# Kernel tuning notes

Hardware: AMD Instinct MI355X
Metric: run time of the kernel (lower is better)

Reference implementation:

```python
import jax, jax.numpy as jnp
import numpy as np

B, H, W, DIM = 32, 56, 56, 192
WSZ = 7
HEADS = 8
DK = 32
DV = 32
INNER_K = HEADS * DK  # 256
INNER_V = HEADS * DV  # 256


def setup_inputs() -> dict:
    key = jax.random.key(0)
    ks = jax.random.split(key, 8)
    s = 0.05
    return {
        "x": jax.random.normal(ks[0], (B, H, W, DIM), jnp.float32),
        "Wq": jax.random.normal(ks[1], (DIM, INNER_K), jnp.float32) * s,
        "Wk": jax.random.normal(ks[2], (DIM, INNER_K), jnp.float32) * s,
        "Wv": jax.random.normal(ks[3], (DIM, INNER_V), jnp.float32) * s,
        "Wlocal": jax.random.normal(ks[4], (3, 3, INNER_V, INNER_V), jnp.float32) * s,
        "b_local": jnp.zeros((INNER_V,), jnp.float32),
        "Wout": jax.random.normal(ks[5], (INNER_V, DIM), jnp.float32) * s,
        "b_out": jnp.zeros((DIM,), jnp.float32),
    }


def _window(t, heads, wsz):
    # (b, H, W, heads*d) -> (b*nx*ny, heads, wsz*wsz, d)
    b, h, w, c = t.shape
    d = c // heads
    nx, ny = h // wsz, w // wsz
    t = t.reshape(b, nx, wsz, ny, wsz, heads, d)
    t = t.transpose(0, 1, 3, 5, 2, 4, 6)
    return t.reshape(b * nx * ny, heads, wsz * wsz, d)


def reference(x, Wq, Wk, Wv, Wlocal, b_local, Wout, b_out):
    scale = DK ** (-0.5)
    # 1x1 convs == per-pixel matmuls
    q = jnp.einsum('bhwc,cd->bhwd', x, Wq)
    k = jnp.einsum('bhwc,cd->bhwd', x, Wk)
    v = jnp.einsum('bhwc,cd->bhwd', x, Wv)
    # 3x3 local interactive conv on v (SAME padding)
    local_out = jax.lax.conv_general_dilated(
        v, Wlocal, window_strides=(1, 1), padding='SAME',
        dimension_numbers=('NHWC', 'HWIO', 'NHWC')) + b_local
    # window partition
    qw = _window(q, HEADS, WSZ)
    kw = _window(k, HEADS, WSZ)
    vw = _window(v, HEADS, WSZ)
    dots = jnp.einsum('bhid,bhjd->bhij', qw, kw) * scale  # (B*nx*ny, heads, 49, 49)
    attn = jax.nn.softmax(dots, axis=-1)
    out = jnp.einsum('bhij,bhjd->bhid', attn, vw)
    # window merge: (b*nx*ny, heads, wsz*wsz, d) -> (b, H, W, heads*d)
    nx, ny = H // WSZ, W // WSZ
    out = out.reshape(B, nx, ny, HEADS, WSZ, WSZ, DV)
    out = out.transpose(0, 1, 4, 2, 5, 3, 6).reshape(B, H, W, HEADS * DV)
    out = out + local_out
    out = jnp.einsum('bhwc,cd->bhwd', out, Wout) + b_out
    return out
```

## Files before the change

kernel.cpp:

```cpp
#include <hip/hip_runtime.h>

typedef unsigned short ushort_t;
typedef __bf16  bf16x8 __attribute__((ext_vector_type(8)));
typedef float   f32x4  __attribute__((ext_vector_type(4)));
typedef unsigned short u16x8 __attribute__((ext_vector_type(8)));

#define MFMA16(a,b,c) __builtin_amdgcn_mfma_f32_16x16x32_bf16((a),(b),(c),0,0,0)
#define WAITVM(N) asm volatile("s_waitcnt vmcnt(" #N ")" ::: "memory")
#define BARRIER() do{ __builtin_amdgcn_s_barrier(); asm volatile("" ::: "memory"); }while(0)

static __device__ __forceinline__ ushort_t f2bf(float f){
  __bf16 h = (__bf16)f;
  return __builtin_bit_cast(ushort_t, h);
}
static __device__ __forceinline__ float bf2f(ushort_t b){
  union{unsigned u; float f;} x; x.u = ((unsigned)b)<<16; return x.f;
}
static __device__ __forceinline__ bf16x8 ldg_bf8u(const ushort_t* p){
  u16x8 r = *(const u16x8*)p;
  return __builtin_bit_cast(bf16x8, r);
}
static __device__ __forceinline__ bf16x8 lds_bf8(const ushort_t* p){
  u16x8 r = *(const u16x8*)p;
  return __builtin_bit_cast(bf16x8, r);
}
static __device__ __forceinline__ void gload_lds16(const ushort_t* g, ushort_t* l){
  __builtin_amdgcn_global_load_lds(
      (const __attribute__((address_space(1))) void*)g,
      (__attribute__((address_space(3))) void*)l, 16, 0, 0);
}

__global__ __launch_bounds__(256) void prep_kernel(
    const float* __restrict__ Wq, const float* __restrict__ Wk,
    const float* __restrict__ Wv, const float* __restrict__ Wl,
    const float* __restrict__ Wo,
    ushort_t* __restrict__ qkvT, ushort_t* __restrict__ wlT,
    ushort_t* __restrict__ woT)
{
  int idx = blockIdx.x*256 + threadIdx.x;
  if(idx < 147456){
    int n = idx/192, kk = idx%192;
    const float* W = (n < 256) ? Wq : ((n < 512) ? Wk : Wv);
    qkvT[idx] = f2bf(W[kk*256 + (n & 255)]);
  } else if(idx < 147456 + 589824){
    int t2 = idx - 147456;
    int j   = t2 & 7;
    int sl  = (t2 >> 3) & 3;
    int col = (t2 >> 5) & 255;
    int ks  = (t2 >> 13) & 7;
    int tap = t2 >> 16;
    int grp = sl ^ ((col>>1)&3);
    int k = ks*32 + grp*8 + j;
    wlT[t2] = f2bf(Wl[((size_t)tap*256 + k)*256 + col]);
  } else if(idx < 737280 + 49152){
    int t3 = idx - 737280;
    int col = t3/256, kk = t3%256;
    woT[t3] = f2bf(Wo[kk*192 + col]);
  }
}

__global__ __launch_bounds__(256,2) void qkvattn_kernel(
    const float* __restrict__ x, const ushort_t* __restrict__ WT,
    ushort_t* __restrict__ vbuf, ushort_t* __restrict__ attnout)
{
  __shared__ ushort_t lds[38912];
  ushort_t* xLds = lds;
  const int tid = threadIdx.x;
  const int w = tid>>6, l = tid&63, lr = l&15, g = l>>4;
  const int bid = blockIdx.x;
  const int win = bid>>1, head = (bid&1)*4 + w;
  const int b = win>>6, rem = win&63, wy = rem>>3, wx = rem&7;
  const size_t base = (size_t)b*3136 + wy*7*56 + wx*7;

  #pragma unroll
  for(int r=0;r<6;++r){
    int c = tid + r*256;
    int row = c/24, cp = c%24;
    if(row < 49){
      int sc = cp ^ (row&7);
      const float* src = x + (base + (row/7)*56 + (row%7))*192 + sc*8;
      float4 f0 = *(const float4*)src;
      float4 f1 = *(const float4*)(src+4);
      u16x8 o;
      o[0]=f2bf(f0.x); o[1]=f2bf(f0.y); o[2]=f2bf(f0.z); o[3]=f2bf(f0.w);
      o[4]=f2bf(f1.x); o[5]=f2bf(f1.y); o[6]=f2bf(f1.z); o[7]=f2bf(f1.w);
      *(u16x8*)&xLds[row*192 + cp*8] = o;
    } else {
      u16x8 z = {0,0,0,0,0,0,0,0};
      *(u16x8*)&xLds[row*192 + cp*8] = z;
    }
  }
  __syncthreads();

  ushort_t* qkBase = lds + 12288 + w*4608;
  ushort_t* vT     = lds + 30720 + w*2048;
  const ushort_t* Wq_ = WT + (size_t)(head*32)*192;
  const ushort_t* Wk_ = WT + (size_t)(256 + head*32)*192;
  const ushort_t* Wv_ = WT + (size_t)(512 + head*32)*192;

  {
    f32x4 aq[4][2], ak[4][2];
    #pragma unroll
    for(int mi=0;mi<4;++mi)
      #pragma unroll
      for(int nj=0;nj<2;++nj){
        f32x4 z={0.f,0.f,0.f,0.f};
        aq[mi][nj]=z; ak[mi][nj]=z;
      }
    #pragma unroll
    for(int ks=0; ks<6; ++ks){
      bf16x8 af[4];
      #pragma unroll
      for(int mi=0;mi<4;++mi){
        int row = mi*16 + lr;
        af[mi] = lds_bf8(&xLds[(row*192 + ks*32 + g*8) ^ ((row&7)<<3)]);
      }
      bf16x8 bq[2], bk[2];
      #pragma unroll
      for(int nj=0;nj<2;++nj){
        size_t off = (size_t)(nj*16+lr)*192 + ks*32 + g*8;
        bq[nj] = ldg_bf8u(Wq_ + off);
        bk[nj] = ldg_bf8u(Wk_ + off);
      }
      #pragma unroll
      for(int nj=0;nj<2;++nj)
        #pragma unroll
        for(int mi=0;mi<4;++mi){
          aq[mi][nj] = MFMA16(af[mi], bq[nj], aq[mi][nj]);
          ak[mi][nj] = MFMA16(af[mi], bk[nj], ak[mi][nj]);
        }
    }
    #pragma unroll
    for(int mi=0;mi<4;++mi)
      #pragma unroll
      for(int nj=0;nj<2;++nj)
        #pragma unroll
        for(int i=0;i<4;++i){
          int row = mi*16 + g*4 + i, col = nj*16 + lr;
          qkBase[row*36 + col]        = f2bf(aq[mi][nj][i]);
          qkBase[2304 + row*36 + col] = f2bf(ak[mi][nj][i]);
        }
  }

  {
    f32x4 av[4][2];
    #pragma unroll
    for(int mi=0;mi<4;++mi)
      #pragma unroll
      for(int nj=0;nj<2;++nj){ f32x4 z={0.f,0.f,0.f,0.f}; av[mi][nj]=z; }
    #pragma unroll
    for(int ks=0; ks<6; ++ks){
      bf16x8 af[4];
      #pragma unroll
      for(int mi=0;mi<4;++mi){
        int row = mi*16 + lr;
        af[mi] = lds_bf8(&xLds[(row*192 + ks*32 + g*8) ^ ((row&7)<<3)]);
      }
      bf16x8 bv[2];
      #pragma unroll
      for(int nj=0;nj<2;++nj)
        bv[nj] = ldg_bf8u(Wv_ + (size_t)(nj*16+lr)*192 + ks*32 + g*8);
      #pragma unroll
      for(int nj=0;nj<2;++nj)
        #pragma unroll
        for(int mi=0;mi<4;++mi)
          av[mi][nj] = MFMA16(af[mi], bv[nj], av[mi][nj]);
    }
    #pragma unroll
    for(int mi=0;mi<4;++mi)
      #pragma unroll
      for(int nj=0;nj<2;++nj)
        #pragma unroll
        for(int i=0;i<4;++i){
          int row = mi*16 + g*4 + i, col = nj*16 + lr;
          ushort_t val = f2bf(av[mi][nj][i]);
          vT[(col*64 + row) ^ ((col&7)<<3)] = val;
          if(row < 49)
            vbuf[(base + (row/7)*56 + (row%7))*256 + head*32 + col] = val;
        }
  }

  f32x4 dot[4][4];
  #pragma unroll
  for(int mi=0;mi<4;++mi)
    #pragma unroll
    for(int nj=0;nj<4;++nj){ f32x4 z={0.f,0.f,0.f,0.f}; dot[mi][nj]=z; }
  bf16x8 qf[4], kf[4];
  #pragma unroll
  for(int t=0;t<4;++t){
    qf[t] = lds_bf8(&qkBase[(t*16+lr)*36 + g*8]);
    kf[t] = lds_bf8(&qkBase[2304 + (t*16+lr)*36 + g*8]);
  }
  #pragma unroll
  for(int mi=0;mi<4;++mi)
    #pragma unroll
    for(int nj=0;nj<4;++nj)
      dot[mi][nj] = MFMA16(qf[mi], kf[nj], dot[mi][nj]);

  const float sc = 0.17677669529663687f * 1.4426950408889634f;
  ushort_t* pl = qkBase;
  #pragma unroll
  for(int mi=0;mi<4;++mi)
    #pragma unroll
    for(int nj=0;nj<4;++nj){
      int col = nj*16 + lr;
      #pragma unroll
      for(int i=0;i<4;++i){
        float e = (col < 49) ? exp2f(dot[mi][nj][i]*sc) : 0.f;
        int row = mi*16 + g*4 + i;
        pl[(row*64 + col) ^ ((row&7)<<3)] = f2bf(e);
      }
    }

  u16x8 ones_u = {0x3f80,0x3f80,0x3f80,0x3f80,0x3f80,0x3f80,0x3f80,0x3f80};
  bf16x8 ones8 = __builtin_bit_cast(bf16x8, ones_u);
  f32x4 o[4][2], rsum[4];
  #pragma unroll
  for(int mi=0;mi<4;++mi){
    f32x4 z={0.f,0.f,0.f,0.f};
    o[mi][0]=z; o[mi][1]=z; rsum[mi]=z;
  }
  #pragma unroll
  for(int ks=0;ks<2;++ks){
    bf16x8 pa[4];
    #pragma unroll
    for(int mi=0;mi<4;++mi){
      int row = mi*16 + lr;
      pa[mi] = lds_bf8(&pl[(row*64 + ks*32 + g*8) ^ ((row&7)<<3)]);
    }
    #pragma unroll
    for(int nj=0;nj<2;++nj){
      int d = nj*16 + lr;
      bf16x8 vb = lds_bf8(&vT[(d*64 + ks*32 + g*8) ^ ((d&7)<<3)]);
      #pragma unroll
      for(int mi=0;mi<4;++mi) o[mi][nj] = MFMA16(pa[mi], vb, o[mi][nj]);
    }
    #pragma unroll
    for(int mi=0;mi<4;++mi) rsum[mi] = MFMA16(pa[mi], ones8, rsum[mi]);
  }
  #pragma unroll
  for(int mi=0;mi<4;++mi){
    #pragma unroll
    for(int i=0;i<4;++i){
      int row = mi*16 + g*4 + i;
      if(row < 49){
        size_t pix = base + (row/7)*56 + (row%7);
        float inv = 1.0f / rsum[mi][i];
        #pragma unroll
        for(int nj=0;nj<2;++nj)
          attnout[pix*256 + head*32 + nj*16 + lr] = f2bf(o[mi][nj][i] * inv);
      }
    }
  }
}

__global__ __launch_bounds__(256,2) void conv_kernel(
    const ushort_t* __restrict__ v, const ushort_t* __restrict__ WlT,
    const float* __restrict__ b_local, ushort_t* __restrict__ local_out)
{
  __shared__ ushort_t aBuf[2][256*32];
  __shared__ ushort_t bBuf[3][256*32];
  const int bid = blockIdx.x;
  const int tile = (bid & 7) * 98 + (bid >> 3);
  const int p0 = tile * 128;
  const int tid = threadIdx.x;
  const int l = tid&63, w=tid>>6, wm=w>>1, wn=w&1, lr=l&15, g=l>>4;

  unsigned maskbits[4];
  int pxloc[4];
  #pragma unroll
  for(int mi=0;mi<4;++mi){
    int p = p0 + wm*64 + mi*16 + lr;
    int rem = p % 3136;
    int y = rem/56, x = rem%56;
    unsigned mb = 0;
    #pragma unroll
    for(int tap=0;tap<9;++tap){
      int dy = tap/3 - 1, dx = tap%3 - 1;
      if(((unsigned)(y+dy) < 56u) && ((unsigned)(x+dx) < 56u)) mb |= (1u<<tap);
    }
    maskbits[mi] = mb;
    pxloc[mi] = wm*64 + mi*16 + lr + 64;
  }

  auto stageA = [&](int ks, ushort_t* dst){
    #pragma unroll
    for(int r=0;r<4;++r){
      int c = tid + r*256;
      int px = c>>2, sl = c&3;
      int px_abs = p0 - 64 + px;
      px_abs = min(max(px_abs, 0), 100351);
      int chunk = sl ^ ((px>>1)&3);
      gload_lds16(v + (size_t)px_abs*256 + ks*32 + chunk*8,
                  dst + (size_t)(r*256 + w*64)*8);
    }
  };
  auto stageB = [&](int ks, int tap, ushort_t* dst){
    const ushort_t* src = WlT + ((size_t)tap*8 + ks)*8192;
    #pragma unroll
    for(int r=0;r<4;++r){
      gload_lds16(src + (size_t)(tid + r*256)*8,
                  dst + (size_t)(r*256 + w*64)*8);
    }
  };

  f32x4 acc[4][8];
  #pragma unroll
  for(int mi=0;mi<4;++mi)
    #pragma unroll
    for(int nj=0;nj<8;++nj){ f32x4 z={0.f,0.f,0.f,0.f}; acc[mi][nj]=z; }

  auto compute = [&](int tap, const ushort_t* aL, const ushort_t* bL){
    int shift = (tap/3 - 1)*56 + (tap%3 - 1);
    bf16x8 af[4];
    #pragma unroll
    for(int mi=0;mi<4;++mi){
      int px = pxloc[mi] + shift;
      int sl = g ^ ((px>>1)&3);
      u16x8 rv = *(const u16x8*)&aL[px*32 + sl*8];
      if(!((maskbits[mi]>>tap)&1)){ u16x8 z={0,0,0,0,0,0,0,0}; rv=z; }
      af[mi] = __builtin_bit_cast(bf16x8, rv);
    }
    __builtin_amdgcn_s_setprio(1);
    #pragma unroll
    for(int nj=0;nj<8;++nj){
      int col = wn*128 + nj*16 + lr;
      int slb = g ^ ((col>>1)&3);
      bf16x8 bfr = lds_bf8(&bL[col*32 + slb*8]);
      #pragma unroll
      for(int mi=0;mi<4;++mi) acc[mi][nj] = MFMA16(af[mi], bfr, acc[mi][nj]);
    }
    __builtin_amdgcn_s_setprio(0);
  };

  stageA(0, aBuf[0]);
  stageB(0, 0, bBuf[0]);
  stageB(0, 1, bBuf[1]);

  for(int ks=0; ks<7; ++ks){
    #pragma unroll
    for(int tap=0; tap<9; ++tap){
      if(tap==1) WAITVM(8); else WAITVM(4);
      BARRIER();
      if(tap==0) stageA(ks+1, aBuf[(ks+1)&1]);
      stageB(ks + (tap+2)/9, (tap+2)%9, bBuf[(tap+2)%3]);
      compute(tap, aBuf[ks&1], bBuf[tap%3]);
    }
  }
  #pragma unroll
  for(int tap=0; tap<9; ++tap){
    if(tap==8) WAITVM(0); else WAITVM(4);
    BARRIER();
    if(tap<7) stageB(7, tap+2, bBuf[(tap+2)%3]);
    compute(tap, aBuf[1], bBuf[tap%3]);
  }

  #pragma unroll
  for(int nj=0;nj<8;++nj){
    int col = wn*128 + nj*16 + lr;
    float bb = b_local[col];
    #pragma unroll
    for(int mi=0;mi<4;++mi)
      #pragma unroll
      for(int i=0;i<4;++i){
        int p = p0 + wm*64 + mi*16 + g*4 + i;
        local_out[(size_t)p*256 + col] = f2bf(acc[mi][nj][i] + bb);
      }
  }
}

__global__ __launch_bounds__(256,4) void outproj_kernel(
    const ushort_t* __restrict__ attnout, const ushort_t* __restrict__ locl,
    const ushort_t* __restrict__ WoT, const float* __restrict__ b_out,
    float* __restrict__ out)
{
  __shared__ ushort_t aLds[64*256];
  const int m0 = blockIdx.x * 64;
  const int tid = threadIdx.x;
  const int l = tid&63, w = tid>>6, lr=l&15, g=l>>4;
  #pragma unroll
  for(int r=0;r<8;++r){
    int c = tid + r*256;
    int row = c>>5, cc = c&31;
    size_t off = (size_t)(m0+row)*256 + cc*8;
    u16x8 a = *(const u16x8*)(attnout + off);
    u16x8 b2 = *(const u16x8*)(locl + off);
    u16x8 o;
    #pragma unroll
    for(int j=0;j<8;++j) o[j] = f2bf(bf2f(a[j]) + bf2f(b2[j]));
    *(u16x8*)&aLds[(row*256 + cc*8) ^ ((row&7)<<3)] = o;
  }
  __syncthreads();

  const ushort_t* Wbase = WoT + (size_t)(w*48)*256;
  f32x4 acc[4][3];
  #pragma unroll
  for(int mi=0;mi<4;++mi)
    #pragma unroll
    for(int nj=0;nj<3;++nj){ f32x4 z={0.f,0.f,0.f,0.f}; acc[mi][nj]=z; }

  #pragma unroll
  for(int ks=0;ks<8;++ks){
    bf16x8 bfr[3];
    #pragma unroll
    for(int nj=0;nj<3;++nj)
      bfr[nj] = ldg_bf8u(Wbase + (size_t)(nj*16+lr)*256 + ks*32 + g*8);
    bf16x8 af[4];
    #pragma unroll
    for(int mi=0;mi<4;++mi){
      int row = mi*16 + lr;
      af[mi] = lds_bf8(&aLds[(row*256 + ks*32 + g*8) ^ ((row&7)<<3)]);
    }
    #pragma unroll
    for(int nj=0;nj<3;++nj)
      #pragma unroll
      for(int mi=0;mi<4;++mi) acc[mi][nj] = MFMA16(af[mi], bfr[nj], acc[mi][nj]);
  }
  #pragma unroll
  for(int nj=0;nj<3;++nj){
    int col = w*48 + nj*16 + lr;
    float bb = b_out[col];
    #pragma unroll
    for(int mi=0;mi<4;++mi)
      #pragma unroll
      for(int i=0;i<4;++i){
        int row = mi*16 + g*4 + i;
        out[(size_t)(m0+row)*192 + col] = acc[mi][nj][i] + bb;
      }
  }
}

extern "C" void kernel_launch(void* const* d_in, const int* in_sizes, int n_in,
                              void* d_out, int out_size, void* d_ws, size_t ws_size,
                              hipStream_t stream)
{
  const float* x  = (const float*)d_in[0];
  const float* Wq = (const float*)d_in[1];
  const float* Wk = (const float*)d_in[2];
  const float* Wv = (const float*)d_in[3];
  const float* Wl = (const float*)d_in[4];
  const float* bl = (const float*)d_in[5];
  const float* Wo = (const float*)d_in[6];
  const float* bo = (const float*)d_in[7];
  float* out = (float*)d_out;
  char* ws = (char*)d_ws;
  ushort_t* attnout = (ushort_t*)(ws);
  ushort_t* vbuf    = (ushort_t*)(ws + 102760448);
  ushort_t* locl    = (ushort_t*)(ws + 205520896);
  ushort_t* qkvT    = (ushort_t*)(ws + 256901120);
  ushort_t* wlT     = (ushort_t*)(ws + 257196032);
  ushort_t* woT     = (ushort_t*)(ws + 258375680);

  prep_kernel<<<3072, 256, 0, stream>>>(Wq, Wk, Wv, Wl, Wo, qkvT, wlT, woT);
  qkvattn_kernel<<<4096, 256, 0, stream>>>(x, qkvT, vbuf, attnout);
  conv_kernel<<<784, 256, 0, stream>>>(vbuf, wlT, bl, locl);
  outproj_kernel<<<1568, 256, 0, stream>>>(attnout, locl, woT, bo, out);
}
```

Before: 323.5 us.

## Pre-convert x to bf16 in prep kernel and load A fragments from global

The fp32-to-bf16 conversion of x moves into the prep kernel, which now writes a bf16 copy of x to workspace. The QKV/attention kernel no longer stages the window into shared memory. Each wave instead loads its MFMA A fragments straight from the bf16 global buffer, clamping padded rows to row 48. This removes the LDS staging, its barrier and about 24KB of LDS per block, and halves the bytes of x each attention block reads. In exchange it adds a full extra write-and-read pass over x, and every wave now fetches x fragments redundantly from global/L2 instead of sharing them through LDS.

```diff
diff --git a/kernel.cpp b/kernel.cpp
--- a/kernel.cpp
+++ b/kernel.cpp
@@ -31,11 +31,12 @@
 }
 
 __global__ __launch_bounds__(256) void prep_kernel(
+    const float* __restrict__ x,
     const float* __restrict__ Wq, const float* __restrict__ Wk,
     const float* __restrict__ Wv, const float* __restrict__ Wl,
     const float* __restrict__ Wo,
     ushort_t* __restrict__ qkvT, ushort_t* __restrict__ wlT,
-    ushort_t* __restrict__ woT)
+    ushort_t* __restrict__ woT, ushort_t* __restrict__ xbf)
 {
   int idx = blockIdx.x*256 + threadIdx.x;
   if(idx < 147456){
@@ -56,15 +57,23 @@
     int t3 = idx - 737280;
     int col = t3/256, kk = t3%256;
     woT[t3] = f2bf(Wo[kk*192 + col]);
+  } else {
+    int c = idx - 786432;
+    const float* src = x + (size_t)c*8;
+    float4 f0 = *(const float4*)src;
+    float4 f1 = *(const float4*)(src+4);
+    u16x8 o;
+    o[0]=f2bf(f0.x); o[1]=f2bf(f0.y); o[2]=f2bf(f0.z); o[3]=f2bf(f0.w);
+    o[4]=f2bf(f1.x); o[5]=f2bf(f1.y); o[6]=f2bf(f1.z); o[7]=f2bf(f1.w);
+    *(u16x8*)&xbf[(size_t)c*8] = o;
   }
 }
 
 __global__ __launch_bounds__(256,2) void qkvattn_kernel(
-    const float* __restrict__ x, const ushort_t* __restrict__ WT,
+    const ushort_t* __restrict__ xbf, const ushort_t* __restrict__ WT,
     ushort_t* __restrict__ vbuf, ushort_t* __restrict__ attnout)
 {
-  __shared__ ushort_t lds[38912];
-  ushort_t* xLds = lds;
+  __shared__ ushort_t lds[26624];
   const int tid = threadIdx.x;
   const int w = tid>>6, l = tid&63, lr = l&15, g = l>>4;
   const int bid = blockIdx.x;
@@ -72,28 +81,15 @@
   const int b = win>>6, rem = win&63, wy = rem>>3, wx = rem&7;
   const size_t base = (size_t)b*3136 + wy*7*56 + wx*7;
 
-  #pragma unroll
-  for(int r=0;r<6;++r){
-    int c = tid + r*256;
-    int row = c/24, cp = c%24;
-    if(row < 49){
-      int sc = cp ^ (row&7);
-      const float* src = x + (base + (row/7)*56 + (row%7))*192 + sc*8;
-      float4 f0 = *(const float4*)src;
-      float4 f1 = *(const float4*)(src+4);
-      u16x8 o;
-      o[0]=f2bf(f0.x); o[1]=f2bf(f0.y); o[2]=f2bf(f0.z); o[3]=f2bf(f0.w);
-      o[4]=f2bf(f1.x); o[5]=f2bf(f1.y); o[6]=f2bf(f1.z); o[7]=f2bf(f1.w);
-      *(u16x8*)&xLds[row*192 + cp*8] = o;
-    } else {
-      u16x8 z = {0,0,0,0,0,0,0,0};
-      *(u16x8*)&xLds[row*192 + cp*8] = z;
-    }
-  }
-  __syncthreads();
-
-  ushort_t* qkBase = lds + 12288 + w*4608;
-  ushort_t* vT     = lds + 30720 + w*2048;
+  const ushort_t* aPtr[4];
+  #pragma unroll
+  for(int mi=0;mi<4;++mi){
+    int row = mi*16 + lr; row = (row > 48) ? 48 : row;
+    aPtr[mi] = xbf + (base + (row/7)*56 + (row%7))*192;
+  }
+
+  ushort_t* qkBase = lds + w*4608;
+  ushort_t* vT     = lds + 18432 + w*2048;
   const ushort_t* Wq_ = WT + (size_t)(head*32)*192;
   const ushort_t* Wk_ = WT + (size_t)(256 + head*32)*192;
   const ushort_t* Wv_ = WT + (size_t)(512 + head*32)*192;
@@ -111,10 +107,7 @@
     for(int ks=0; ks<6; ++ks){
       bf16x8 af[4];
       #pragma unroll
-      for(int mi=0;mi<4;++mi){
-        int row = mi*16 + lr;
-        af[mi] = lds_bf8(&xLds[(row*192 + ks*32 + g*8) ^ ((row&7)<<3)]);
-      }
+      for(int mi=0;mi<4;++mi) af[mi] = ldg_bf8u(aPtr[mi] + ks*32 + g*8);
       bf16x8 bq[2], bk[2];
       #pragma unroll
       for(int nj=0;nj<2;++nj){
@@ -152,10 +145,7 @@
     for(int ks=0; ks<6; ++ks){
       bf16x8 af[4];
       #pragma unroll
-      for(int mi=0;mi<4;++mi){
-        int row = mi*16 + lr;
-        af[mi] = lds_bf8(&xLds[(row*192 + ks*32 + g*8) ^ ((row&7)<<3)]);
-      }
+      for(int mi=0;mi<4;++mi) af[mi] = ldg_bf8u(aPtr[mi] + ks*32 + g*8);
       bf16x8 bv[2];
       #pragma unroll
       for(int nj=0;nj<2;++nj)
@@ -445,14 +435,15 @@
   float* out = (float*)d_out;
   char* ws = (char*)d_ws;
   ushort_t* attnout = (ushort_t*)(ws);
+  ushort_t* xbf     = (ushort_t*)(ws + 51380224);
   ushort_t* vbuf    = (ushort_t*)(ws + 102760448);
   ushort_t* locl    = (ushort_t*)(ws + 205520896);
   ushort_t* qkvT    = (ushort_t*)(ws + 256901120);
   ushort_t* wlT     = (ushort_t*)(ws + 257196032);
   ushort_t* woT     = (ushort_t*)(ws + 258375680);
 
-  prep_kernel<<<3072, 256, 0, stream>>>(Wq, Wk, Wv, Wl, Wo, qkvT, wlT, woT);
-  qkvattn_kernel<<<4096, 256, 0, stream>>>(x, qkvT, vbuf, attnout);
+  prep_kernel<<<12480, 256, 0, stream>>>(x, Wq, Wk, Wv, Wl, Wo, qkvT, wlT, woT, xbf);
+  qkvattn_kernel<<<4096, 256, 0, stream>>>(xbf, qkvT, vbuf, attnout);
   conv_kernel<<<784, 256, 0, stream>>>(vbuf, wlT, bl, locl);
   outproj_kernel<<<1568, 256, 0, stream>>>(attnout, locl, woT, bo, out);
 }
```

Measured after the change: 341.9 us. 5.7% more time.

## Fuse output projection into local conv kernel via shared-memory epilogue

Applied to the files above, without the earlier changes.

Merges the conv and out-projection kernels. Each conv block writes its 128x256 local output tile to shared memory, adds the attention output tile, then runs the Wout GEMM from shared memory and writes the final fp32 result. This removes the bf16 local_out round trip through global memory and one kernel launch. In exchange the conv kernel holds more accumulator registers at occupancy 2 and has a serial epilogue with extra barriers.

```diff
diff --git a/kernel.cpp b/kernel.cpp
--- a/kernel.cpp
+++ b/kernel.cpp
@@ -254,12 +254,16 @@
   }
 }
 
-__global__ __launch_bounds__(256,2) void conv_kernel(
+__global__ __launch_bounds__(256,2) void conv_outproj_kernel(
     const ushort_t* __restrict__ v, const ushort_t* __restrict__ WlT,
-    const float* __restrict__ b_local, ushort_t* __restrict__ local_out)
+    const ushort_t* __restrict__ attnout, const float* __restrict__ b_local,
+    const ushort_t* __restrict__ woT, const float* __restrict__ b_out,
+    float* __restrict__ out)
 {
-  __shared__ ushort_t aBuf[2][256*32];
-  __shared__ ushort_t bBuf[3][256*32];
+  __shared__ ushort_t sh[40960];
+  ushort_t* aBuf0 = sh;
+  ushort_t* aBuf1 = sh + 8192;
+  ushort_t* bBufs = sh + 16384;
   const int bid = blockIdx.x;
   const int tile = (bid & 7) * 98 + (bid >> 3);
   const int p0 = tile * 128;
@@ -333,28 +337,30 @@
     __builtin_amdgcn_s_setprio(0);
   };
 
-  stageA(0, aBuf[0]);
-  stageB(0, 0, bBuf[0]);
-  stageB(0, 1, bBuf[1]);
+  stageA(0, aBuf0);
+  stageB(0, 0, bBufs);
+  stageB(0, 1, bBufs + 8192);
 
   for(int ks=0; ks<7; ++ks){
     #pragma unroll
     for(int tap=0; tap<9; ++tap){
       if(tap==1) WAITVM(8); else WAITVM(4);
       BARRIER();
-      if(tap==0) stageA(ks+1, aBuf[(ks+1)&1]);
-      stageB(ks + (tap+2)/9, (tap+2)%9, bBuf[(tap+2)%3]);
-      compute(tap, aBuf[ks&1], bBuf[tap%3]);
+      if(tap==0) stageA(ks+1, (ks&1) ? aBuf0 : aBuf1);
+      stageB(ks + (tap+2)/9, (tap+2)%9, bBufs + ((tap+2)%3)*8192);
+      compute(tap, (ks&1) ? aBuf1 : aBuf0, bBufs + (tap%3)*8192);
     }
   }
   #pragma unroll
   for(int tap=0; tap<9; ++tap){
     if(tap==8) WAITVM(0); else WAITVM(4);
     BARRIER();
-    if(tap<7) stageB(7, tap+2, bBuf[(tap+2)%3]);
-    compute(tap, aBuf[1], bBuf[tap%3]);
-  }
-
+    if(tap<7) stageB(7, tap+2, bBufs + ((tap+2)%3)*8192);
+    compute(tap, aBuf1, bBufs + (tap%3)*8192);
+  }
+
+  BARRIER();
+  ushort_t* sum = sh;
   #pragma unroll
   for(int nj=0;nj<8;++nj){
     int col = wn*128 + nj*16 + lr;
@@ -363,69 +369,56 @@
     for(int mi=0;mi<4;++mi)
       #pragma unroll
       for(int i=0;i<4;++i){
-        int p = p0 + wm*64 + mi*16 + g*4 + i;
-        local_out[(size_t)p*256 + col] = f2bf(acc[mi][nj][i] + bb);
-      }
-  }
-}
-
-__global__ __launch_bounds__(256,4) void outproj_kernel(
-    const ushort_t* __restrict__ attnout, const ushort_t* __restrict__ locl,
-    const ushort_t* __restrict__ WoT, const float* __restrict__ b_out,
-    float* __restrict__ out)
-{
-  __shared__ ushort_t aLds[64*256];
-  const int m0 = blockIdx.x * 64;
-  const int tid = threadIdx.x;
-  const int l = tid&63, w = tid>>6, lr=l&15, g=l>>4;
-  #pragma unroll
-  for(int r=0;r<8;++r){
+        int row = wm*64 + mi*16 + g*4 + i;
+        sum[(row*256 + col) ^ ((row&7)<<3)] = f2bf(acc[mi][nj][i] + bb);
+      }
+  }
+  BARRIER();
+  #pragma unroll
+  for(int r=0;r<16;++r){
     int c = tid + r*256;
     int row = c>>5, cc = c&31;
-    size_t off = (size_t)(m0+row)*256 + cc*8;
-    u16x8 a = *(const u16x8*)(attnout + off);
-    u16x8 b2 = *(const u16x8*)(locl + off);
+    u16x8 a = *(const u16x8*)(attnout + (size_t)(p0+row)*256 + cc*8);
+    ushort_t* sp = &sum[(row*256 + cc*8) ^ ((row&7)<<3)];
+    u16x8 s = *(u16x8*)sp;
     u16x8 o;
     #pragma unroll
-    for(int j=0;j<8;++j) o[j] = f2bf(bf2f(a[j]) + bf2f(b2[j]));
-    *(u16x8*)&aLds[(row*256 + cc*8) ^ ((row&7)<<3)] = o;
-  }
-  __syncthreads();
-
-  const ushort_t* Wbase = WoT + (size_t)(w*48)*256;
-  f32x4 acc[4][3];
+    for(int j=0;j<8;++j) o[j] = f2bf(bf2f(s[j]) + bf2f(a[j]));
+    *(u16x8*)sp = o;
+  }
+  BARRIER();
+  f32x4 acc2[4][6];
   #pragma unroll
   for(int mi=0;mi<4;++mi)
     #pragma unroll
-    for(int nj=0;nj<3;++nj){ f32x4 z={0.f,0.f,0.f,0.f}; acc[mi][nj]=z; }
-
+    for(int nj=0;nj<6;++nj){ f32x4 z={0.f,0.f,0.f,0.f}; acc2[mi][nj]=z; }
   #pragma unroll
   for(int ks=0;ks<8;++ks){
-    bf16x8 bfr[3];
-    #pragma unroll
-    for(int nj=0;nj<3;++nj)
-      bfr[nj] = ldg_bf8u(Wbase + (size_t)(nj*16+lr)*256 + ks*32 + g*8);
+    bf16x8 bfr[6];
+    #pragma unroll
+    for(int nj=0;nj<6;++nj)
+      bfr[nj] = ldg_bf8u(woT + (size_t)(wn*96 + nj*16 + lr)*256 + ks*32 + g*8);
     bf16x8 af[4];
     #pragma unroll
     for(int mi=0;mi<4;++mi){
-      int row = mi*16 + lr;
-      af[mi] = lds_bf8(&aLds[(row*256 + ks*32 + g*8) ^ ((row&7)<<3)]);
-    }
-    #pragma unroll
-    for(int nj=0;nj<3;++nj)
-      #pragma unroll
-      for(int mi=0;mi<4;++mi) acc[mi][nj] = MFMA16(af[mi], bfr[nj], acc[mi][nj]);
-  }
-  #pragma unroll
-  for(int nj=0;nj<3;++nj){
-    int col = w*48 + nj*16 + lr;
+      int row = wm*64 + mi*16 + lr;
+      af[mi] = lds_bf8(&sum[(row*256 + ks*32 + g*8) ^ ((row&7)<<3)]);
+    }
+    #pragma unroll
+    for(int nj=0;nj<6;++nj)
+      #pragma unroll
+      for(int mi=0;mi<4;++mi) acc2[mi][nj] = MFMA16(af[mi], bfr[nj], acc2[mi][nj]);
+  }
+  #pragma unroll
+  for(int nj=0;nj<6;++nj){
+    int col = wn*96 + nj*16 + lr;
     float bb = b_out[col];
     #pragma unroll
     for(int mi=0;mi<4;++mi)
       #pragma unroll
       for(int i=0;i<4;++i){
-        int row = mi*16 + g*4 + i;
-        out[(size_t)(m0+row)*192 + col] = acc[mi][nj][i] + bb;
+        int row = wm*64 + mi*16 + g*4 + i;
+        out[(size_t)(p0+row)*192 + col] = acc2[mi][nj][i] + bb;
       }
   }
 }
@@ -446,13 +439,11 @@
   char* ws = (char*)d_ws;
   ushort_t* attnout = (ushort_t*)(ws);
   ushort_t* vbuf    = (ushort_t*)(ws + 102760448);
-  ushort_t* locl    = (ushort_t*)(ws + 205520896);
   ushort_t* qkvT    = (ushort_t*)(ws + 256901120);
   ushort_t* wlT     = (ushort_t*)(ws + 257196032);
   ushort_t* woT     = (ushort_t*)(ws + 258375680);
 
   prep_kernel<<<3072, 256, 0, stream>>>(Wq, Wk, Wv, Wl, Wo, qkvT, wlT, woT);
   qkvattn_kernel<<<4096, 256, 0, stream>>>(x, qkvT, vbuf, attnout);
-  conv_kernel<<<784, 256, 0, stream>>>(vbuf, wlT, bl, locl);
-  outproj_kernel<<<1568, 256, 0, stream>>>(attnout, locl, woT, bo, out);
-}
+  conv_outproj_kernel<<<784, 256, 0, stream>>>(vbuf, wlT, attnout, bl, woT, bo, out);
+}
```

Result: slower. 336.2 us (+3.9%).
